# Kernel tuning notes

Hardware: AMD Instinct MI355X
Metric: run time of the kernel (lower is better)

## Reference

```python
import jax, jax.numpy as jnp
import numpy as np

D_MODEL = 1024
N_HEADS = 16
D_FF = 4096
EPS = 1e-5


def setup_inputs() -> dict:
    key = jax.random.key(0)
    ks = jax.random.split(key, 16)
    s = 1.0 / np.sqrt(D_MODEL)
    x = jax.random.normal(ks[0], (4, 2048, D_MODEL), dtype=jnp.float32)
    Wq = jax.random.normal(ks[1], (D_MODEL, D_MODEL), jnp.float32) * s
    bq = jnp.zeros((D_MODEL,), jnp.float32)
    Wk = jax.random.normal(ks[2], (D_MODEL, D_MODEL), jnp.float32) * s
    bk = jnp.zeros((D_MODEL,), jnp.float32)
    Wv = jax.random.normal(ks[3], (D_MODEL, D_MODEL), jnp.float32) * s
    bv = jnp.zeros((D_MODEL,), jnp.float32)
    Wo = jax.random.normal(ks[4], (D_MODEL, D_MODEL), jnp.float32) * s
    bo = jnp.zeros((D_MODEL,), jnp.float32)
    W1 = jax.random.normal(ks[5], (D_MODEL, D_FF), jnp.float32) * s
    b1 = jnp.zeros((D_FF,), jnp.float32)
    W2 = jax.random.normal(ks[6], (D_FF, D_MODEL), jnp.float32) * (1.0 / np.sqrt(D_FF))
    b2 = jnp.zeros((D_MODEL,), jnp.float32)
    g1 = jnp.ones((D_MODEL,), jnp.float32)
    beta1 = jnp.zeros((D_MODEL,), jnp.float32)
    g2 = jnp.ones((D_MODEL,), jnp.float32)
    beta2 = jnp.zeros((D_MODEL,), jnp.float32)
    return {"x": x, "Wq": Wq, "bq": bq, "Wk": Wk, "bk": bk, "Wv": Wv, "bv": bv,
            "Wo": Wo, "bo": bo, "W1": W1, "b1": b1, "W2": W2, "b2": b2,
            "g1": g1, "beta1": beta1, "g2": g2, "beta2": beta2}


def _layernorm(x, g, b):
    mu = jnp.mean(x, axis=-1, keepdims=True)
    var = jnp.mean(jnp.square(x - mu), axis=-1, keepdims=True)
    return (x - mu) * jax.lax.rsqrt(var + EPS) * g + b


def reference(x, Wq, bq, Wk, bk, Wv, bv, Wo, bo, W1, b1, W2, b2, g1, beta1, g2, beta2):
    B, S, D = x.shape
    H, dk = N_HEADS, D // N_HEADS
    # QKV projections -> [B, H, S, dk]
    q = (x @ Wq + bq).reshape(B, S, H, dk).transpose(0, 2, 1, 3)
    k = (x @ Wk + bk).reshape(B, S, H, dk).transpose(0, 2, 1, 3)
    v = (x @ Wv + bv).reshape(B, S, H, dk).transpose(0, 2, 1, 3)
    scores = jnp.einsum('bhqd,bhkd->bhqk', q, k) / np.sqrt(dk)  # [B,H,S,S]
    attn = jax.nn.softmax(scores, axis=-1)
    out = jnp.einsum('bhqk,bhkd->bhqd', attn, v)
    out = out.transpose(0, 2, 1, 3).reshape(B, S, D) @ Wo + bo
    x2 = _layernorm(x + out, g1, beta1)
    ff = jax.nn.relu(x2 @ W1 + b1) @ W2 + b2
    return _layernorm(x2 + ff, g2, beta2)
```

## Files before the change

kernel.cpp:

```cpp
#include <hip/hip_runtime.h>
#include <math.h>
#include <stdint.h>


#define D_MODEL 1024
#define N_HEADS 16
#define DKH     64
#define D_FF    4096
#define BATCH   4
#define SEQ     2048
#define NTOK    (BATCH * SEQ)
#define LN_EPS  1e-5f
#define QKV_LD  3072
#define QSCALE  0.18033688011112042f

typedef unsigned short u16;
typedef __attribute__((ext_vector_type(8))) short bf16x8;
typedef __attribute__((ext_vector_type(4))) float f32x4;
typedef __attribute__((ext_vector_type(16))) float f32x16;

__device__ __forceinline__ u16 f2bf(float f) {
    union { float f; uint32_t u; } c; c.f = f;
    return (u16)((c.u + 0x7FFFu + ((c.u >> 16) & 1u)) >> 16);
}
__device__ __forceinline__ float bf2f(u16 h) {
    union { uint32_t u; float f; } c; c.u = ((uint32_t)h) << 16;
    return c.f;
}

__device__ __forceinline__ void gload16(const u16* g, u16* lds) {
    __builtin_amdgcn_global_load_lds(
        (const __attribute__((address_space(1))) uint32_t*)g,
        (__attribute__((address_space(3))) uint32_t*)(uintptr_t)lds,
        16, 0, 0);
}

__device__ __forceinline__ void store_out(float* p, float v) { *p = v; }
__device__ __forceinline__ void store_out(u16* p, float v)   { *p = f2bf(v); }

template <int MODE, typename OutT>
__global__ __launch_bounds__(256, 2) void gemm_bf16_kernel(
    const u16* __restrict__ A, const u16* __restrict__ Bt,
    const float* __restrict__ bias, const float* __restrict__ bias2,
    const float* __restrict__ bias3, OutT* __restrict__ C,
    int M, int N, int K)
{
    __shared__ u16 Alds[128 * 32];
    __shared__ u16 Blds[128 * 32];

    const int tid  = threadIdx.x;
    const int wave = tid >> 6;
    const int lane = tid & 63;
    const int lo   = lane & 15;
    const int hi   = lane >> 4;
    const int m0   = blockIdx.y << 7;
    const int n0   = blockIdx.x << 7;
    const int wr   = wave >> 1;
    const int wc   = wave & 1;

    const int srow = wave * 32 + (lane >> 2);
    const int scol = (lane & 3) * 8;
    const u16* Ag = A  + (size_t)(m0 + srow) * K + scol;
    const u16* Bg = Bt + (size_t)(n0 + srow) * K + scol;
    u16* AldsW = Alds + wave * 1024;
    u16* BldsW = Blds + wave * 1024;

    f32x4 acc[4][4];
#pragma unroll
    for (int i = 0; i < 4; ++i)
#pragma unroll
        for (int j = 0; j < 4; ++j)
#pragma unroll
            for (int r = 0; r < 4; ++r) acc[i][j][r] = 0.f;

    for (int k0 = 0; k0 < K; k0 += 32) {
        __syncthreads();
        gload16(Ag + k0,                  AldsW);
        gload16(Ag + k0 + 16 * (size_t)K, AldsW + 512);
        gload16(Bg + k0,                  BldsW);
        gload16(Bg + k0 + 16 * (size_t)K, BldsW + 512);
        __syncthreads();

        bf16x8 a[4], b[4];
#pragma unroll
        for (int i = 0; i < 4; ++i) {
            a[i] = *(const bf16x8*)&Alds[(wr * 64 + i * 16 + lo) * 32 + hi * 8];
            b[i] = *(const bf16x8*)&Blds[(wc * 64 + i * 16 + lo) * 32 + hi * 8];
        }
#pragma unroll
        for (int i = 0; i < 4; ++i)
#pragma unroll
            for (int j = 0; j < 4; ++j)
                acc[i][j] = __builtin_amdgcn_mfma_f32_16x16x32_bf16(
                                a[i], b[j], acc[i][j], 0, 0, 0);
    }

    const int crow = m0 + wr * 64 + hi * 4;
    const int ccol = n0 + wc * 64 + lo;
#pragma unroll
    for (int j = 0; j < 4; ++j) {
        const int col = ccol + j * 16;
        float bj;
        float sc = 1.0f;
        if (MODE == 2) {
            bj = (col < 1024) ? bias[col]
               : (col < 2048) ? bias2[col - 1024] : bias3[col - 2048];
            if (col < 1024) sc = QSCALE;
        } else {
            bj = bias[col];
        }
#pragma unroll
        for (int i = 0; i < 4; ++i)
#pragma unroll
            for (int r = 0; r < 4; ++r) {
                float v = acc[i][j][r] + bj;
                if (MODE == 1) v = fmaxf(v, 0.f);
                if (MODE == 2) v *= sc;
                store_out(&C[(size_t)(crow + i * 16 + r) * N + col], v);
            }
    }
}

__global__ __launch_bounds__(256, 3) void attn_mfma_kernel(
    const u16* __restrict__ QKV, u16* __restrict__ O)
{
    __shared__ u16 Klds[64 * 64];
    __shared__ u16 Vlds[64 * 64];

    const int tid  = threadIdx.x;
    const int wave = tid >> 6;
    const int lane = tid & 63;
    const int l31  = lane & 31;
    const int hi5  = lane >> 5;
    const int b    = blockIdx.x >> 4;
    const int h    = blockIdx.x & 15;
    const int q0   = blockIdx.y * 128 + wave * 32;
    const size_t rowb = (size_t)b * SEQ * QKV_LD + (size_t)h * DKH;
    const u16* Qg = QKV + rowb;
    const u16* Kg = QKV + rowb + 1024;
    const u16* Vg = QKV + rowb + 2048;

    bf16x8 qf[4];
#pragma unroll
    for (int f = 0; f < 4; ++f)
        qf[f] = *(const bf16x8*)&Qg[(size_t)(q0 + l31) * QKV_LD + 16 * f + 8 * hi5];

    f32x16 oacc[2];
#pragma unroll
    for (int g = 0; g < 2; ++g)
#pragma unroll
        for (int r = 0; r < 16; ++r) oacc[g][r] = 0.f;
    float mrun = -1e30f, lrun = 0.f;

    const int krow = wave * 8 + (lane >> 3);
    const int kchk = ((lane & 7) ^ ((lane >> 3) & 7)) << 3;
    u16* kdst = Klds + wave * 512;

    const int vdk0 = (tid & 15) * 4;
    const int vkv  = (tid >> 4) * 4;
    const int vchk = vkv >> 3;
    const int vsub = vkv & 7;

    for (int kv0 = 0; kv0 < SEQ; kv0 += 64) {
        __syncthreads();
        gload16(Kg + (size_t)(kv0 + krow) * QKV_LD + kchk,      kdst);
        gload16(Kg + (size_t)(kv0 + krow + 32) * QKV_LD + kchk, kdst + 32 * 64);
        alignas(8) u16 e[4][4];
#pragma unroll
        for (int i = 0; i < 4; ++i)
            *(uint2*)e[i] = *(const uint2*)&Vg[(size_t)(kv0 + vkv + i) * QKV_LD + vdk0];
#pragma unroll
        for (int j = 0; j < 4; ++j) {
            alignas(8) u16 w4[4] = { e[0][j], e[1][j], e[2][j], e[3][j] };
            const int row = vdk0 + j;
            *(uint2*)&Vlds[row * 64 + ((vchk ^ (row & 7)) << 3) + vsub] = *(const uint2*)w4;
        }
        __syncthreads();

        f32x16 s0, s1;
#pragma unroll
        for (int r = 0; r < 16; ++r) { s0[r] = 0.f; s1[r] = 0.f; }
#pragma unroll
        for (int f = 0; f < 4; ++f) {
            const int rc = ((2 * f + hi5) ^ (l31 & 7)) << 3;
            const bf16x8 ka = *(const bf16x8*)&Klds[l31 * 64 + rc];
            const bf16x8 kb = *(const bf16x8*)&Klds[(32 + l31) * 64 + rc];
            s0 = __builtin_amdgcn_mfma_f32_32x32x16_bf16(ka, qf[f], s0, 0, 0, 0);
            s1 = __builtin_amdgcn_mfma_f32_32x32x16_bf16(kb, qf[f], s1, 0, 0, 0);
        }

        float tm = s0[0];
#pragma unroll
        for (int r = 1; r < 16; ++r) tm = fmaxf(tm, s0[r]);
#pragma unroll
        for (int r = 0; r < 16; ++r) tm = fmaxf(tm, s1[r]);
        tm = fmaxf(tm, __shfl_xor(tm, 32, 64));
        if (__any(tm > mrun + 8.0f)) {
            const float mnew = fmaxf(mrun, tm);
            const float corr = exp2f(mrun - mnew);
            lrun *= corr;
#pragma unroll
            for (int g = 0; g < 2; ++g)
#pragma unroll
                for (int r = 0; r < 16; ++r) oacc[g][r] *= corr;
            mrun = mnew;
        }
        float ls = 0.f;
#pragma unroll
        for (int r = 0; r < 16; ++r) { s0[r] = exp2f(s0[r] - mrun); ls += s0[r]; }
#pragma unroll
        for (int r = 0; r < 16; ++r) { s1[r] = exp2f(s1[r] - mrun); ls += s1[r]; }
        lrun += ls;

        auto mkfrag = [&](float a0, float a1, float a2, float a3,
                          float a4, float a5, float a6, float a7) -> bf16x8 {
            uint32_t A, B, C, D;
            asm("v_cvt_pk_bf16_f32 %0, %1, %2" : "=v"(A) : "v"(a0), "v"(a1));
            asm("v_cvt_pk_bf16_f32 %0, %1, %2" : "=v"(B) : "v"(a2), "v"(a3));
            asm("v_cvt_pk_bf16_f32 %0, %1, %2" : "=v"(C) : "v"(a4), "v"(a5));
            asm("v_cvt_pk_bf16_f32 %0, %1, %2" : "=v"(D) : "v"(a6), "v"(a7));
            const uint32_t Ax = (uint32_t)__shfl_xor((int)A, 32, 64);
            const uint32_t Bx = (uint32_t)__shfl_xor((int)B, 32, 64);
            const uint32_t Cx = (uint32_t)__shfl_xor((int)C, 32, 64);
            const uint32_t Dx = (uint32_t)__shfl_xor((int)D, 32, 64);
            union { uint32_t w[4]; bf16x8 v; } u;
            u.w[0] = hi5 ? Cx : A;
            u.w[1] = hi5 ? Dx : B;
            u.w[2] = hi5 ? C  : Ax;
            u.w[3] = hi5 ? D  : Bx;
            return u.v;
        };
        bf16x8 pb0 = mkfrag(s0[0], s0[1], s0[2],  s0[3],  s0[4],  s0[5],  s0[6],  s0[7]);
        bf16x8 pb1 = mkfrag(s0[8], s0[9], s0[10], s0[11], s0[12], s0[13], s0[14], s0[15]);
        bf16x8 pb2 = mkfrag(s1[0], s1[1], s1[2],  s1[3],  s1[4],  s1[5],  s1[6],  s1[7]);
        bf16x8 pb3 = mkfrag(s1[8], s1[9], s1[10], s1[11], s1[12], s1[13], s1[14], s1[15]);

#pragma unroll
        for (int f = 0; f < 4; ++f) {
            const bf16x8 pf = (f == 0) ? pb0 : (f == 1) ? pb1 : (f == 2) ? pb2 : pb3;
            const int rc = ((2 * f + hi5) ^ (l31 & 7)) << 3;
            const bf16x8 va = *(const bf16x8*)&Vlds[l31 * 64 + rc];
            const bf16x8 vb = *(const bf16x8*)&Vlds[(32 + l31) * 64 + rc];
            oacc[0] = __builtin_amdgcn_mfma_f32_32x32x16_bf16(va, pf, oacc[0], 0, 0, 0);
            oacc[1] = __builtin_amdgcn_mfma_f32_32x32x16_bf16(vb, pf, oacc[1], 0, 0, 0);
        }
    }

    lrun += __shfl_xor(lrun, 32, 64);
    const float inv = 1.0f / lrun;
    u16* Orow = O + (size_t)b * SEQ * D_MODEL + (size_t)(q0 + l31) * D_MODEL + h * DKH;
#pragma unroll
    for (int g = 0; g < 2; ++g)
#pragma unroll
        for (int rp = 0; rp < 8; ++rp) {
            const int r = rp * 2;
            const float v0 = oacc[g][r] * inv;
            const float v1 = oacc[g][r + 1] * inv;
            uint32_t pk;
            asm("v_cvt_pk_bf16_f32 %0, %1, %2" : "=v"(pk) : "v"(v0), "v"(v1));
            const int d = 32 * g + (r & 3) + 8 * (r >> 2) + 4 * hi5;
            *(uint32_t*)&Orow[d] = pk;
        }
}

__global__ __launch_bounds__(256) void transpose_w_kernel(
    const float* __restrict__ W, u16* __restrict__ Wt, int K, int N)
{
    __shared__ float t[32][33];
    const int n0 = blockIdx.x << 5;
    const int k0 = blockIdx.y << 5;
    const int tx = threadIdx.x & 31;
    const int ty = threadIdx.x >> 5;
#pragma unroll
    for (int i = 0; i < 4; ++i)
        t[ty + i * 8][tx] = W[(size_t)(k0 + ty + i * 8) * N + n0 + tx];
    __syncthreads();
#pragma unroll
    for (int i = 0; i < 4; ++i)
        Wt[(size_t)(n0 + ty + i * 8) * K + k0 + tx] = f2bf(t[tx][ty + i * 8]);
}

__global__ __launch_bounds__(256) void cvt_kernel(
    const float* __restrict__ src, u16* __restrict__ dst)
{
    const size_t i = ((size_t)blockIdx.x * 256 + threadIdx.x) * 8;
    const float4 a = *(const float4*)&src[i];
    const float4 b = *(const float4*)&src[i + 4];
    alignas(16) u16 e[8] = { f2bf(a.x), f2bf(a.y), f2bf(a.z), f2bf(a.w),
                             f2bf(b.x), f2bf(b.y), f2bf(b.z), f2bf(b.w) };
    *(int4*)&dst[i] = *(const int4*)e;
}

__device__ __forceinline__ float4 ld4(const float* p) { return *(const float4*)p; }
__device__ __forceinline__ float4 ld4(const u16* p) {
    alignas(8) u16 e[4];
    *(uint2*)e = *(const uint2*)p;
    return make_float4(bf2f(e[0]), bf2f(e[1]), bf2f(e[2]), bf2f(e[3]));
}
__device__ __forceinline__ void st4(float* p, float4 v) { *(float4*)p = v; }
__device__ __forceinline__ void st4(u16* p, float4 v) {
    alignas(8) u16 e[4] = { f2bf(v.x), f2bf(v.y), f2bf(v.z), f2bf(v.w) };
    *(uint2*)p = *(const uint2*)e;
}

template <typename XT, typename YT, typename OT>
__global__ __launch_bounds__(256) void add_ln_kernel(
    const XT* __restrict__ X, const YT* __restrict__ Y,
    const float* __restrict__ gamma, const float* __restrict__ beta,
    OT* __restrict__ Out)
{
    const int row = blockIdx.x;
    const int i0  = threadIdx.x << 2;
    const float4 xv = ld4(X + (size_t)row * D_MODEL + i0);
    const float4 yv = ld4(Y + (size_t)row * D_MODEL + i0);
    const float4 v  = make_float4(xv.x + yv.x, xv.y + yv.y, xv.z + yv.z, xv.w + yv.w);

    float s1 = v.x + v.y + v.z + v.w;
    float s2 = v.x * v.x + v.y * v.y + v.z * v.z + v.w * v.w;
#pragma unroll
    for (int off = 32; off > 0; off >>= 1) {
        s1 += __shfl_xor(s1, off, 64);
        s2 += __shfl_xor(s2, off, 64);
    }
    __shared__ float red[8];
    const int wid = threadIdx.x >> 6;
    if ((threadIdx.x & 63) == 0) { red[wid] = s1; red[wid + 4] = s2; }
    __syncthreads();
    s1 = red[0] + red[1] + red[2] + red[3];
    s2 = red[4] + red[5] + red[6] + red[7];

    const float mu   = s1 * (1.0f / D_MODEL);
    const float var  = s2 * (1.0f / D_MODEL) - mu * mu;
    const float rstd = rsqrtf(var + LN_EPS);

    const float4 g  = *(const float4*)(gamma + i0);
    const float4 bb = *(const float4*)(beta + i0);
    float4 ov;
    ov.x = (v.x - mu) * rstd * g.x + bb.x;
    ov.y = (v.y - mu) * rstd * g.y + bb.y;
    ov.z = (v.z - mu) * rstd * g.z + bb.z;
    ov.w = (v.w - mu) * rstd * g.w + bb.w;
    st4(Out + (size_t)row * D_MODEL + i0, ov);
}

extern "C" void kernel_launch(void* const* d_in, const int* in_sizes, int n_in,
                              void* d_out, int out_size, void* d_ws, size_t ws_size,
                              hipStream_t stream)
{
    const float* x     = (const float*)d_in[0];
    const float* Wq    = (const float*)d_in[1];
    const float* bq    = (const float*)d_in[2];
    const float* Wk    = (const float*)d_in[3];
    const float* bk    = (const float*)d_in[4];
    const float* Wv    = (const float*)d_in[5];
    const float* bv    = (const float*)d_in[6];
    const float* Wo    = (const float*)d_in[7];
    const float* bo    = (const float*)d_in[8];
    const float* W1    = (const float*)d_in[9];
    const float* b1    = (const float*)d_in[10];
    const float* W2    = (const float*)d_in[11];
    const float* b2    = (const float*)d_in[12];
    const float* g1    = (const float*)d_in[13];
    const float* beta1 = (const float*)d_in[14];
    const float* g2    = (const float*)d_in[15];
    const float* beta2 = (const float*)d_in[16];
    float* out = (float*)d_out;

    const size_t TOKD = (size_t)NTOK * D_MODEL;
    u16* xb    = (u16*)d_ws;
    u16* wqkvT = xb + TOKD;
    u16* woT   = wqkvT + (size_t)3 * D_MODEL * D_MODEL;
    u16* w1T   = woT + (size_t)D_MODEL * D_MODEL;
    u16* w2T   = w1T + (size_t)D_MODEL * D_FF;
    u16* qkv   = w2T + (size_t)D_FF * D_MODEL;
    u16* ctx   = qkv + (size_t)NTOK * QKV_LD;
    u16* y1    = ctx + TOKD;
    u16* x2    = y1;
    u16* h1    = qkv;

    const dim3 blk(256);

    cvt_kernel<<<dim3(TOKD / 2048), blk, 0, stream>>>(x, xb);
    transpose_w_kernel<<<dim3(D_MODEL / 32, D_MODEL / 32), blk, 0, stream>>>(Wq, wqkvT, D_MODEL, D_MODEL);
    transpose_w_kernel<<<dim3(D_MODEL / 32, D_MODEL / 32), blk, 0, stream>>>(Wk, wqkvT + (size_t)D_MODEL * D_MODEL, D_MODEL, D_MODEL);
    transpose_w_kernel<<<dim3(D_MODEL / 32, D_MODEL / 32), blk, 0, stream>>>(Wv, wqkvT + (size_t)2 * D_MODEL * D_MODEL, D_MODEL, D_MODEL);
    transpose_w_kernel<<<dim3(D_MODEL / 32, D_MODEL / 32), blk, 0, stream>>>(Wo, woT, D_MODEL, D_MODEL);
    transpose_w_kernel<<<dim3(D_FF / 32,    D_MODEL / 32), blk, 0, stream>>>(W1, w1T, D_MODEL, D_FF);
    transpose_w_kernel<<<dim3(D_MODEL / 32, D_FF / 32),    blk, 0, stream>>>(W2, w2T, D_FF, D_MODEL);

    gemm_bf16_kernel<2, u16><<<dim3(QKV_LD / 128, NTOK / 128), blk, 0, stream>>>(
        xb, wqkvT, bq, bk, bv, qkv, NTOK, QKV_LD, D_MODEL);

    attn_mfma_kernel<<<dim3(BATCH * N_HEADS, SEQ / 128), blk, 0, stream>>>(qkv, ctx);

    gemm_bf16_kernel<0, u16><<<dim3(D_MODEL / 128, NTOK / 128), blk, 0, stream>>>(
        ctx, woT, bo, bo, bo, y1, NTOK, D_MODEL, D_MODEL);

    add_ln_kernel<float, u16, u16><<<dim3(NTOK), blk, 0, stream>>>(x, y1, g1, beta1, x2);

    gemm_bf16_kernel<1, u16><<<dim3(D_FF / 128, NTOK / 128), blk, 0, stream>>>(
        x2, w1T, b1, b1, b1, h1, NTOK, D_FF, D_MODEL);
    gemm_bf16_kernel<0, float><<<dim3(D_MODEL / 128, NTOK / 128), blk, 0, stream>>>(
        h1, w2T, b2, b2, b2, out, NTOK, D_MODEL, D_FF);

    add_ln_kernel<u16, float, float><<<dim3(NTOK), blk, 0, stream>>>(x2, out, g2, beta2, out);

    (void)in_sizes; (void)n_in; (void)out_size; (void)ws_size;
}
```

Measured before the change: 450.8 us.

## Pipeline GEMM with multi-buffered LDS, 512-thread 128x256 tiles, permlane32 swap in attention

Replaces the GEMM with a 512-thread kernel computing 128x256 tiles at K-step 64. A is triple-buffered and B double-buffered in swizzled LDS, and loads are issued ahead with a single vmcnt wait plus barrier per iteration instead of two syncthreads. The aim is to overlap global loads with MFMA work and cut barrier and LDS bank-conflict stalls. The attention kernel also swaps four shfl_xor calls and selects for v_permlane32_swap when building P fragments. The larger LDS footprint lowers occupancy, and the hand-placed waitcnt and wraparound prefetch indices are risky.

```diff
diff --git a/kernel.cpp b/kernel.cpp
--- a/kernel.cpp
+++ b/kernel.cpp
@@ -39,31 +39,46 @@
 __device__ __forceinline__ void store_out(u16* p, float v)   { *p = f2bf(v); }
 
 template <int MODE, typename OutT>
-__global__ __launch_bounds__(256, 2) void gemm_bf16_kernel(
+__global__ __launch_bounds__(512) void gemm_pipe_kernel(
     const u16* __restrict__ A, const u16* __restrict__ Bt,
     const float* __restrict__ bias, const float* __restrict__ bias2,
     const float* __restrict__ bias3, OutT* __restrict__ C,
     int M, int N, int K)
 {
-    __shared__ u16 Alds[128 * 32];
-    __shared__ u16 Blds[128 * 32];
+    __shared__ u16 lds[3 * 8192 + 2 * 16384];
 
     const int tid  = threadIdx.x;
     const int wave = tid >> 6;
     const int lane = tid & 63;
     const int lo   = lane & 15;
     const int hi   = lane >> 4;
+    const int wr   = wave >> 2;
+    const int wc   = wave & 3;
     const int m0   = blockIdx.y << 7;
-    const int n0   = blockIdx.x << 7;
-    const int wr   = wave >> 1;
-    const int wc   = wave & 1;
-
-    const int srow = wave * 32 + (lane >> 2);
-    const int scol = (lane & 3) * 8;
-    const u16* Ag = A  + (size_t)(m0 + srow) * K + scol;
-    const u16* Bg = Bt + (size_t)(n0 + srow) * K + scol;
-    u16* AldsW = Alds + wave * 1024;
-    u16* BldsW = Blds + wave * 1024;
+    const int n0   = blockIdx.x << 8;
+    const int NT   = K >> 6;
+
+    const int srow = lane >> 3;
+    const int schk = (lane & 7) ^ srow;
+    const u16* AgS = A  + (size_t)(m0 + wave * 16 + srow) * K + schk * 8;
+    const u16* BgS = Bt + (size_t)(n0 + wave * 32 + srow) * K + schk * 8;
+    u16* AdS = lds + wave * 1024;
+    u16* BdS = lds + 24576 + wave * 2048;
+
+    auto stageA = [&](int kt, int buf) {
+        const u16* g = AgS + kt * 64;
+        u16* d = AdS + buf * 8192;
+#pragma unroll
+        for (int q = 0; q < 2; ++q)
+            gload16(g + (size_t)q * 8 * K, d + q * 512);
+    };
+    auto stageB = [&](int kt, int buf) {
+        const u16* g = BgS + kt * 64;
+        u16* d = BdS + buf * 16384;
+#pragma unroll
+        for (int q = 0; q < 4; ++q)
+            gload16(g + (size_t)q * 8 * K, d + q * 512);
+    };
 
     f32x4 acc[4][4];
 #pragma unroll
@@ -73,33 +88,52 @@
 #pragma unroll
             for (int r = 0; r < 4; ++r) acc[i][j][r] = 0.f;
 
-    for (int k0 = 0; k0 < K; k0 += 32) {
-        __syncthreads();
-        gload16(Ag + k0,                  AldsW);
-        gload16(Ag + k0 + 16 * (size_t)K, AldsW + 512);
-        gload16(Bg + k0,                  BldsW);
-        gload16(Bg + k0 + 16 * (size_t)K, BldsW + 512);
-        __syncthreads();
-
-        bf16x8 a[4], b[4];
-#pragma unroll
-        for (int i = 0; i < 4; ++i) {
-            a[i] = *(const bf16x8*)&Alds[(wr * 64 + i * 16 + lo) * 32 + hi * 8];
-            b[i] = *(const bf16x8*)&Blds[(wc * 64 + i * 16 + lo) * 32 + hi * 8];
-        }
-#pragma unroll
-        for (int i = 0; i < 4; ++i)
-#pragma unroll
-            for (int j = 0; j < 4; ++j)
-                acc[i][j] = __builtin_amdgcn_mfma_f32_16x16x32_bf16(
-                                a[i], b[j], acc[i][j], 0, 0, 0);
+    stageA(0, 0);
+    stageB(0, 0);
+    stageA(1, 1);
+    __builtin_amdgcn_sched_barrier(0);
+    asm volatile("s_waitcnt vmcnt(2)" ::: "memory");
+    __builtin_amdgcn_s_barrier();
+    __builtin_amdgcn_sched_barrier(0);
+
+    for (int t = 0; t < NT; ++t) {
+        int tb = t + 1; if (tb >= NT) tb = 0;
+        int ta = t + 2; if (ta >= NT) ta -= NT;
+        stageB(tb, (t + 1) & 1);
+        stageA(ta, (t + 2) % 3);
+
+        const u16* Ab = lds + (t % 3) * 8192;
+        const u16* Bb = lds + 24576 + (t & 1) * 16384;
+#pragma unroll
+        for (int ks = 0; ks < 2; ++ks) {
+            bf16x8 a[4], b[4];
+#pragma unroll
+            for (int i = 0; i < 4; ++i) {
+                const int ar = wr * 64 + i * 16 + lo;
+                a[i] = *(const bf16x8*)&Ab[ar * 64 + (((ks * 4 + hi) ^ (ar & 7)) << 3)];
+                const int br = wc * 64 + i * 16 + lo;
+                b[i] = *(const bf16x8*)&Bb[br * 64 + (((ks * 4 + hi) ^ (br & 7)) << 3)];
+            }
+            __builtin_amdgcn_s_setprio(1);
+#pragma unroll
+            for (int i = 0; i < 4; ++i)
+#pragma unroll
+                for (int j = 0; j < 4; ++j)
+                    acc[i][j] = __builtin_amdgcn_mfma_f32_16x16x32_bf16(
+                                    a[i], b[j], acc[i][j], 0, 0, 0);
+            __builtin_amdgcn_s_setprio(0);
+        }
+        __builtin_amdgcn_sched_barrier(0);
+        asm volatile("s_waitcnt vmcnt(2)" ::: "memory");
+        __builtin_amdgcn_s_barrier();
+        __builtin_amdgcn_sched_barrier(0);
     }
 
-    const int crow = m0 + wr * 64 + hi * 4;
-    const int ccol = n0 + wc * 64 + lo;
+    const int crow0 = m0 + wr * 64 + hi * 4;
+    const int ccol0 = n0 + wc * 64 + lo;
 #pragma unroll
     for (int j = 0; j < 4; ++j) {
-        const int col = ccol + j * 16;
+        const int col = ccol0 + j * 16;
         float bj;
         float sc = 1.0f;
         if (MODE == 2) {
@@ -116,7 +150,7 @@
                 float v = acc[i][j][r] + bj;
                 if (MODE == 1) v = fmaxf(v, 0.f);
                 if (MODE == 2) v *= sc;
-                store_out(&C[(size_t)(crow + i * 16 + r) * N + col], v);
+                store_out(&C[(size_t)(crow0 + i * 16 + r) * N + col], v);
             }
     }
 }
@@ -153,7 +187,7 @@
     float mrun = -1e30f, lrun = 0.f;
 
     const int krow = wave * 8 + (lane >> 3);
-    const int kchk = ((lane & 7) ^ ((lane >> 3) & 7)) << 3;
+    const int kchk = ((lane & 7) ^ (lane >> 3)) << 3;
     u16* kdst = Klds + wave * 512;
 
     const int vdk0 = (tid & 15) * 4;
@@ -216,18 +250,13 @@
                           float a4, float a5, float a6, float a7) -> bf16x8 {
             uint32_t A, B, C, D;
             asm("v_cvt_pk_bf16_f32 %0, %1, %2" : "=v"(A) : "v"(a0), "v"(a1));
-            asm("v_cvt_pk_bf16_f32 %0, %1, %2" : "=v"(B) : "v"(a2), "v"(a3));
-            asm("v_cvt_pk_bf16_f32 %0, %1, %2" : "=v"(C) : "v"(a4), "v"(a5));
+            asm("v_cvt_pk_bf16_f32 %0, %1, %2" : "=v"(C) : "v"(a2), "v"(a3));
+            asm("v_cvt_pk_bf16_f32 %0, %1, %2" : "=v"(B) : "v"(a4), "v"(a5));
             asm("v_cvt_pk_bf16_f32 %0, %1, %2" : "=v"(D) : "v"(a6), "v"(a7));
-            const uint32_t Ax = (uint32_t)__shfl_xor((int)A, 32, 64);
-            const uint32_t Bx = (uint32_t)__shfl_xor((int)B, 32, 64);
-            const uint32_t Cx = (uint32_t)__shfl_xor((int)C, 32, 64);
-            const uint32_t Dx = (uint32_t)__shfl_xor((int)D, 32, 64);
+            asm volatile("v_permlane32_swap_b32 %0, %1" : "+v"(A), "+v"(B));
+            asm volatile("v_permlane32_swap_b32 %0, %1" : "+v"(C), "+v"(D));
             union { uint32_t w[4]; bf16x8 v; } u;
-            u.w[0] = hi5 ? Cx : A;
-            u.w[1] = hi5 ? Dx : B;
-            u.w[2] = hi5 ? C  : Ax;
-            u.w[3] = hi5 ? D  : Bx;
+            u.w[0] = A; u.w[1] = C; u.w[2] = B; u.w[3] = D;
             return u.v;
         };
         bf16x8 pb0 = mkfrag(s0[0], s0[1], s0[2],  s0[3],  s0[4],  s0[5],  s0[6],  s0[7]);
@@ -379,6 +408,7 @@
     u16* h1    = qkv;
 
     const dim3 blk(256);
+    const dim3 blk5(512);
 
     cvt_kernel<<<dim3(TOKD / 2048), blk, 0, stream>>>(x, xb);
     transpose_w_kernel<<<dim3(D_MODEL / 32, D_MODEL / 32), blk, 0, stream>>>(Wq, wqkvT, D_MODEL, D_MODEL);
@@ -388,19 +418,19 @@
     transpose_w_kernel<<<dim3(D_FF / 32,    D_MODEL / 32), blk, 0, stream>>>(W1, w1T, D_MODEL, D_FF);
     transpose_w_kernel<<<dim3(D_MODEL / 32, D_FF / 32),    blk, 0, stream>>>(W2, w2T, D_FF, D_MODEL);
 
-    gemm_bf16_kernel<2, u16><<<dim3(QKV_LD / 128, NTOK / 128), blk, 0, stream>>>(
+    gemm_pipe_kernel<2, u16><<<dim3(QKV_LD / 256, NTOK / 128), blk5, 0, stream>>>(
         xb, wqkvT, bq, bk, bv, qkv, NTOK, QKV_LD, D_MODEL);
 
     attn_mfma_kernel<<<dim3(BATCH * N_HEADS, SEQ / 128), blk, 0, stream>>>(qkv, ctx);
 
-    gemm_bf16_kernel<0, u16><<<dim3(D_MODEL / 128, NTOK / 128), blk, 0, stream>>>(
+    gemm_pipe_kernel<0, u16><<<dim3(D_MODEL / 256, NTOK / 128), blk5, 0, stream>>>(
         ctx, woT, bo, bo, bo, y1, NTOK, D_MODEL, D_MODEL);
 
     add_ln_kernel<float, u16, u16><<<dim3(NTOK), blk, 0, stream>>>(x, y1, g1, beta1, x2);
 
-    gemm_bf16_kernel<1, u16><<<dim3(D_FF / 128, NTOK / 128), blk, 0, stream>>>(
+    gemm_pipe_kernel<1, u16><<<dim3(D_FF / 256, NTOK / 128), blk5, 0, stream>>>(
         x2, w1T, b1, b1, b1, h1, NTOK, D_FF, D_MODEL);
-    gemm_bf16_kernel<0, float><<<dim3(D_MODEL / 128, NTOK / 128), blk, 0, stream>>>(
+    gemm_pipe_kernel<0, float><<<dim3(D_MODEL / 256, NTOK / 128), blk5, 0, stream>>>(
         h1, w2T, b2, b2, b2, out, NTOK, D_MODEL, D_FF);
 
     add_ln_kernel<u16, float, float><<<dim3(NTOK), blk, 0, stream>>>(x2, out, g2, beta2, out);
```

Result: faster. 414.2 us (-8.1%).
